# Kernel optimization log

Measured on AMD Instinct MI355X. Metric: run time of the kernel, lower is better.

## Reference

```python
import jax, jax.numpy as jnp
import numpy as np

N, T, D = 32, 64, 16
F = 512  # object_classes == feature dim after object_fc


def _gcn(x, adj, W, b):
    # Kipf GraphConvolution: adj @ (x @ W) + b
    return adj @ (x @ W) + b


def _norm_adj(a):
    d = jnp.sum(a, axis=1) ** -0.5
    return a * d[:, None] * d[None, :]


def _per_graph(x, gc1_W, gc1_b, gc2_W, gc2_b, gc3_W, gc3_b, gc4_W, gc4_b):
    # x: [D, F]
    # graph_generator / adj2: softmax-style similarity adjacency with D^{-1/2} norm
    s = x @ x.T                                   # [D, D]
    a = jnp.exp(s - jnp.max(s, axis=1, keepdims=True))
    adj = _norm_adj(a)
    # branch 1
    x1 = jax.nn.relu(_gcn(x, adj, gc1_W, gc1_b))
    x1 = _gcn(x1, adj, gc2_W, gc2_b)
    # branch 2 (adj_hat2 identical construction from x)
    y2 = jax.nn.relu(_gcn(x, adj, gc3_W, gc3_b))  # [D, 32]
    y22 = y2 @ y2.T
    nrm = jnp.sqrt(jnp.sum(y22 * y22, axis=1, keepdims=True))  # torch.norm(y22, 2, dim=1)
    adj3 = 1.0 + y22 / (nrm @ nrm.T)
    adj_hat3 = _norm_adj(adj3)
    y2 = _gcn(y2, adj_hat3, gc4_W, gc4_b)
    return (x1 + y2) * 0.5


def setup_inputs() -> dict:
    key = jax.random.key(0)
    ks = jax.random.split(key, 12)
    s = 0.02
    return {
        "object_raw": jax.random.normal(ks[0], (N * T * D, F), jnp.float32),
        "action_raw": jax.random.normal(ks[1], (N * T, F), jnp.float32),
        "W_obj": jax.random.normal(ks[2], (F, 512), jnp.float32) * s,
        "b_obj": jnp.zeros((512,), jnp.float32),
        "W_act": jax.random.normal(ks[3], (F, 512), jnp.float32) * s,
        "b_act": jnp.zeros((512,), jnp.float32),
        "gc1_W": jax.random.normal(ks[4], (512, 32), jnp.float32) * s,
        "gc1_b": jnp.zeros((32,), jnp.float32),
        "gc2_W": jax.random.normal(ks[5], (32, 512), jnp.float32) * s,
        "gc2_b": jnp.zeros((512,), jnp.float32),
        "gc3_W": jax.random.normal(ks[6], (512, 32), jnp.float32) * s,
        "gc3_b": jnp.zeros((32,), jnp.float32),
        "gc4_W": jax.random.normal(ks[7], (32, 512), jnp.float32) * s,
        "gc4_b": jnp.zeros((512,), jnp.float32),
        "fc1_W": jax.random.normal(ks[8], (512, 1024), jnp.float32) * s,
        "fc1_b": jnp.zeros((1024,), jnp.float32),
        "clf_W": jax.random.normal(ks[9], (1024, 500), jnp.float32) * s,
        "clf_b": jnp.zeros((500,), jnp.float32),
    }


def reference(object_raw, action_raw, W_obj, b_obj, W_act, b_act,
              gc1_W, gc1_b, gc2_W, gc2_b, gc3_W, gc3_b, gc4_W, gc4_b,
              fc1_W, fc1_b, clf_W, clf_b):
    obj = jax.nn.relu(object_raw @ W_obj + b_obj).reshape(N * T, D, 512)
    act = jax.nn.relu(action_raw @ W_act + b_act)           # [N*T, 512]
    obj = obj.at[:, D // 2].set(act)                         # overwrite middle frame
    graph = jax.vmap(lambda x: _per_graph(x, gc1_W, gc1_b, gc2_W, gc2_b,
                                          gc3_W, gc3_b, gc4_W, gc4_b))(obj)
    g = graph.reshape(N, T, D, 512).mean(axis=2)
    o = obj.reshape(N, T, D, 512).mean(axis=2)
    feat = (o + g) * 0.5                                     # graph_fusion == 'mean'
    c = jax.nn.relu(feat)                                    # dropout = identity (eval)
    c = jax.nn.relu(c @ fc1_W + fc1_b)
    out = (c @ clf_W + clf_b).mean(axis=1)                   # mean over T -> [N, 500]
    return out
```

## Files before the change

kernel.cpp:

```cpp
#include <hip/hip_runtime.h>
#include <hip/hip_bf16.h>

using ushort_t = unsigned short;
using f32x4  = __attribute__((ext_vector_type(4))) float;
using short8 = __attribute__((ext_vector_type(8))) short;

__device__ __forceinline__ float bflo(unsigned p) {
    union { unsigned u; float f; } x; x.u = p << 16; return x.f;
}
__device__ __forceinline__ float bfhi(unsigned p) {
    union { unsigned u; float f; } x; x.u = p & 0xffff0000u; return x.f;
}
__device__ __forceinline__ ushort_t f2bf(float f) {
    __hip_bfloat16 h = __float2bfloat16(f);
    return *(ushort_t*)&h;
}
__device__ __forceinline__ unsigned pk2bf(float lo, float hi) {
    __hip_bfloat162 h = __float22bfloat162_rn({lo, hi});
    return *(unsigned*)&h;
}

typedef __attribute__((address_space(1))) void glb_void;
typedef __attribute__((address_space(3))) void lds_void;
__device__ __forceinline__ void dma16(const void* g, void* l) {
    __builtin_amdgcn_global_load_lds((glb_void*)(unsigned long long)(uintptr_t)g,
                                     (lds_void*)(unsigned)(uintptr_t)l, 16, 0, 0);
}

__device__ __forceinline__ void tr_tile(const float* __restrict__ S, ushort_t* __restrict__ D,
                                        int K, int N, int Npad, int bx, int by,
                                        int tx, int ty, float* tile )
{
    const int k0 = by * 32, n0 = bx * 32;
#pragma unroll
    for (int r = 0; r < 4; r++) {
        const int k = k0 + ty + r * 8, n = n0 + tx;
        tile[(ty + r * 8) * 33 + tx] = (k < K && n < N) ? S[(size_t)k * N + n] : 0.f;
    }
    __syncthreads();
#pragma unroll
    for (int r = 0; r < 4; r++) {
        const int n = n0 + ty + r * 8, k = k0 + tx;
        if (n < Npad && k < K) D[(size_t)n * K + k] = f2bf(tile[tx * 33 + ty + r * 8]);
    }
}

__global__ __launch_bounds__(256)
void prep_weights(const float* __restrict__ Wobj, ushort_t* __restrict__ WobjT,
                  const float* __restrict__ Wact, ushort_t* __restrict__ WactT,
                  const float* __restrict__ fc1W, ushort_t* __restrict__ fc1T,
                  const float* __restrict__ clfW, ushort_t* __restrict__ clfT,
                  const float* __restrict__ gc1W, ushort_t* __restrict__ W1t,
                  const float* __restrict__ gc3W, ushort_t* __restrict__ W3t,
                  const float* __restrict__ gc2W, ushort_t* __restrict__ W2bf,
                  const float* __restrict__ gc4W, ushort_t* __restrict__ W4bf)
{
    __shared__ float tile[32 * 33];
    const int b = blockIdx.x;
    const int t = threadIdx.x;
    const int tx = t & 31, ty = t >> 5;

    if (b < 1568) {
        const float* S; ushort_t* D; int K, N, Npad, nt, l;
        if      (b < 256)  { S = Wobj; D = WobjT; K = 512;  N = 512;  Npad = 512;  nt = 16; l = b; }
        else if (b < 512)  { S = Wact; D = WactT; K = 512;  N = 512;  Npad = 512;  nt = 16; l = b - 256; }
        else if (b < 1024) { S = fc1W; D = fc1T;  K = 512;  N = 1024; Npad = 1024; nt = 32; l = b - 512; }
        else if (b < 1536) { S = clfW; D = clfT;  K = 1024; N = 500;  Npad = 512;  nt = 16; l = b - 1024; }
        else if (b < 1552) { S = gc1W; D = W1t;   K = 512;  N = 32;   Npad = 32;   nt = 1;  l = b - 1536; }
        else               { S = gc3W; D = W3t;   K = 512;  N = 32;   Npad = 32;   nt = 1;  l = b - 1552; }
        tr_tile(S, D, K, N, Npad, l % nt, l / nt, tx, ty, tile);
    } else {
        const float* S = (b < 1576) ? gc2W : gc4W;
        ushort_t* D    = (b < 1576) ? W2bf : W4bf;
        const int i = (b < 1576 ? b - 1568 : b - 1576) * 256 + t;
        const float4 x = ((const float4*)S)[2 * i];
        const float4 y = ((const float4*)S)[2 * i + 1];
        unsigned r[4] = { pk2bf(x.x, x.y), pk2bf(x.z, x.w), pk2bf(y.x, y.y), pk2bf(y.z, y.w) };
        ((uint4*)D)[i] = *(uint4*)r;
    }
}

__device__ __forceinline__ void store_out(ushort_t* C, size_t idx, float v) { C[idx] = f2bf(v); }
__device__ __forceinline__ void store_out(float* C, size_t idx, float v)    { C[idx] = v; }

template<int RELU, typename AT, typename OT>
__device__ __forceinline__ void gemm_core(
    const AT* __restrict__ A, const ushort_t* __restrict__ Bt,
    const float* __restrict__ bias, OT* __restrict__ C,
    int N, int K, int Nb, int row_mul, int row_add, int bm, int bn, int skip8,
    char* AsRaw, ushort_t* Bs)
{
    const int t = threadIdx.x;
    const int lane = t & 63, w = t >> 6;
    const int mb = (w & 1) * 64, nb = (w >> 1) * 64;
    const int fr = lane & 15, fq = lane >> 4;

    f32x4 acc[16];
#pragma unroll
    for (int i = 0; i < 16; i++) acc[i] = (f32x4){0.f, 0.f, 0.f, 0.f};

    const int brow = lane >> 2, bk = lane & 3;
    const int klog = bk ^ ((brow >> 1) & 3);
    const int arow = lane >> 3, ag = lane & 7;

    for (int k0 = 0; k0 < K; k0 += 32) {
        __syncthreads();
        if constexpr (sizeof(AT) == 4) {
#pragma unroll
            for (int i = 0; i < 4; i++) {
                const int grp = w * 4 + i;
                const int row = grp * 8 + arow;
                const int gl = ag ^ (row & 7);
                dma16((const float*)A + (size_t)(bm + row) * K + k0 + gl * 4,
                      AsRaw + grp * 1024);
            }
        } else {
#pragma unroll
            for (int i = 0; i < 2; i++) {
                const int grp = w * 2 + i;
                const int row = grp * 16 + brow;
                dma16((const ushort_t*)A + (size_t)(bm + row) * K + k0 + klog * 8,
                      (ushort_t*)AsRaw + grp * 512);
            }
        }
#pragma unroll
        for (int i = 0; i < 2; i++) {
            const int grp = w * 2 + i;
            const int row = grp * 16 + brow;
            dma16(Bt + (size_t)(bn + row) * K + k0 + klog * 8, Bs + grp * 512);
        }
        __syncthreads();

        short8 af[4], bf[4];
        if constexpr (sizeof(AT) == 4) {
#pragma unroll
            for (int i = 0; i < 4; i++) {
                const int row = mb + i * 16 + fr;
                const float* base = (const float*)AsRaw + row * 32;
                const f32x4 p0 = *(const f32x4*)(base + (((2 * fq)     ^ (fr & 7)) * 4));
                const f32x4 p1 = *(const f32x4*)(base + (((2 * fq + 1) ^ (fr & 7)) * 4));
                unsigned rr[4] = { pk2bf(p0.x, p0.y), pk2bf(p0.z, p0.w),
                                   pk2bf(p1.x, p1.y), pk2bf(p1.z, p1.w) };
                af[i] = *(short8*)rr;
            }
        } else {
#pragma unroll
            for (int i = 0; i < 4; i++) {
                const int row = mb + i * 16 + fr;
                af[i] = *(const short8*)((const ushort_t*)AsRaw + row * 32 + (fq ^ ((fr >> 1) & 3)) * 8);
            }
        }
#pragma unroll
        for (int j = 0; j < 4; j++) {
            const int row = nb + j * 16 + fr;
            bf[j] = *(const short8*)(Bs + row * 32 + (fq ^ ((fr >> 1) & 3)) * 8);
        }
#pragma unroll
        for (int i = 0; i < 4; i++)
#pragma unroll
            for (int j = 0; j < 4; j++)
                acc[i * 4 + j] = __builtin_amdgcn_mfma_f32_16x16x32_bf16(
                    af[i], bf[j], acc[i * 4 + j], 0, 0, 0);
    }

#pragma unroll
    for (int j = 0; j < 4; j++) {
        const int n = bn + nb + j * 16 + fr;
        const float bv = (n < Nb) ? bias[n] : 0.f;
#pragma unroll
        for (int i = 0; i < 4; i++) {
            const f32x4 a = acc[i * 4 + j];
#pragma unroll
            for (int r = 0; r < 4; r++) {
                if (skip8 && (fq * 4 + r) == 8) continue;
                const int m = bm + mb + i * 16 + fq * 4 + r;
                float v = a[r] + bv;
                if (RELU) v = fmaxf(v, 0.f);
                store_out(C, ((size_t)m * row_mul + row_add) * (size_t)N + n, v);
            }
        }
    }
}

__global__ __launch_bounds__(256)
void gemm_objact(const float* __restrict__ Ao, const ushort_t* __restrict__ Bo,
                 const float* __restrict__ bo,
                 const float* __restrict__ Aa, const ushort_t* __restrict__ Ba,
                 const float* __restrict__ ba, ushort_t* __restrict__ C)
{
    __shared__ __align__(16) char     AsRaw[128 * 32 * 4];
    __shared__ __align__(16) ushort_t Bs[128 * 32];
    if (blockIdx.y < 256)
        gemm_core<1, float, ushort_t>(Ao, Bo, bo, C, 512, 512, 512, 1, 0,
                                      blockIdx.y * 128, blockIdx.x * 128, 1, AsRaw, Bs);
    else
        gemm_core<1, float, ushort_t>(Aa, Ba, ba, C, 512, 512, 512, 16, 8,
                                      (blockIdx.y - 256) * 128, blockIdx.x * 128, 0, AsRaw, Bs);
}

template<int RELU, typename AT, typename OT>
__global__ __launch_bounds__(256)
void gemm_dma(const AT* __restrict__ A, const ushort_t* __restrict__ Bt,
              const float* __restrict__ bias, OT* __restrict__ C,
              int N, int K, int Nb, int row_mul, int row_add)
{
    __shared__ __align__(16) char     AsRaw[128 * 32 * sizeof(AT)];
    __shared__ __align__(16) ushort_t Bs[128 * 32];
    gemm_core<RELU, AT, OT>(A, Bt, bias, C, N, K, Nb, row_mul, row_add,
                            blockIdx.y * 128, blockIdx.x * 128, 0, AsRaw, Bs);
}

__global__ __launch_bounds__(64)
void graph_mfma(const ushort_t* __restrict__ obj,
                const ushort_t* __restrict__ W1t, const float* __restrict__ b1,
                const ushort_t* __restrict__ W2b, const float* __restrict__ b2,
                const ushort_t* __restrict__ W3t, const float* __restrict__ b3,
                const ushort_t* __restrict__ W4b, const float* __restrict__ b4,
                ushort_t* __restrict__ cbuf)
{
    __shared__ float ssb[16 * 17];
    __shared__ float adjt[16 * 20];
    __shared__ float t1s[16 * 36];
    __shared__ float t3s[16 * 36];
    __shared__ float x1s[16 * 36];
    __shared__ float y2s[16 * 36];
    __shared__ float y22s[16 * 17];
    __shared__ float a3t[16 * 20];
    __shared__ float dv[16], dv3[16], nrm[16], cA[16], cA3[16];
    __shared__ float zc1[32], zc4[32];

    const int lane = threadIdx.x;
    const int r = lane & 15, fq = lane >> 4;
    const ushort_t* xg = obj + (size_t)blockIdx.x * 8192;

    short8 xf[16];
#pragma unroll
    for (int kk = 0; kk < 16; kk++)
        xf[kk] = *(const short8*)(xg + r * 512 + kk * 32 + fq * 8);

    f32x4 sacc = (f32x4){0.f, 0.f, 0.f, 0.f};
#pragma unroll
    for (int kk = 0; kk < 16; kk++)
        sacc = __builtin_amdgcn_mfma_f32_16x16x32_bf16(xf[kk], xf[kk], sacc, 0, 0, 0);

    f32x4 a10 = (f32x4){0.f,0.f,0.f,0.f}, a11 = a10, a30 = a10, a31 = a10;
#pragma unroll
    for (int kk = 0; kk < 16; kk++) {
        const short8 w10 = *(const short8*)(W1t + (size_t)(r)      * 512 + kk * 32 + fq * 8);
        const short8 w11 = *(const short8*)(W1t + (size_t)(16 + r) * 512 + kk * 32 + fq * 8);
        const short8 w30 = *(const short8*)(W3t + (size_t)(r)      * 512 + kk * 32 + fq * 8);
        const short8 w31 = *(const short8*)(W3t + (size_t)(16 + r) * 512 + kk * 32 + fq * 8);
        a10 = __builtin_amdgcn_mfma_f32_16x16x32_bf16(xf[kk], w10, a10, 0, 0, 0);
        a11 = __builtin_amdgcn_mfma_f32_16x16x32_bf16(xf[kk], w11, a11, 0, 0, 0);
        a30 = __builtin_amdgcn_mfma_f32_16x16x32_bf16(xf[kk], w30, a30, 0, 0, 0);
        a31 = __builtin_amdgcn_mfma_f32_16x16x32_bf16(xf[kk], w31, a31, 0, 0, 0);
    }

#pragma unroll
    for (int i = 0; i < 4; i++) {
        const int m = fq * 4 + i;
        ssb[m * 17 + r] = sacc[i];
        t1s[m * 36 + r]      = a10[i];
        t1s[m * 36 + 16 + r] = a11[i];
        t3s[m * 36 + r]      = a30[i];
        t3s[m * 36 + 16 + r] = a31[i];
    }
    __syncthreads();

    if (lane < 16) {
        float m = ssb[lane * 17];
#pragma unroll
        for (int j = 1; j < 16; j++) m = fmaxf(m, ssb[lane * 17 + j]);
        float s = 0.f;
#pragma unroll
        for (int j = 0; j < 16; j++) {
            const float e = expf(ssb[lane * 17 + j] - m);
            ssb[lane * 17 + j] = e; s += e;
        }
        dv[lane] = rsqrtf(s);
    }
    __syncthreads();

    {
        const float di = dv[r];
#pragma unroll
        for (int p = 0; p < 4; p++) {
            const int j = fq * 4 + p;
            adjt[j * 20 + r] = ssb[r * 17 + j] * di * dv[j];
        }
    }
    __syncthreads();

    if (lane < 16) {
        float s = 0.f;
#pragma unroll
        for (int i = 0; i < 16; i++) s += adjt[lane * 20 + i];
        cA[lane] = s;
    }

    {
        const int c = lane & 31, hi = lane >> 5;
        const float bb1 = b1[c], bb3 = b3[c];
        float ax[8], ay[8];
#pragma unroll
        for (int i = 0; i < 8; i++) { ax[i] = bb1; ay[i] = bb3; }
#pragma unroll
        for (int j = 0; j < 16; j++) {
            const float t1v = t1s[j * 36 + c], t3v = t3s[j * 36 + c];
            const float4 p = *(const float4*)&adjt[j * 20 + hi * 8];
            const float4 q = *(const float4*)&adjt[j * 20 + hi * 8 + 4];
            ax[0] = fmaf(p.x, t1v, ax[0]); ax[1] = fmaf(p.y, t1v, ax[1]);
            ax[2] = fmaf(p.z, t1v, ax[2]); ax[3] = fmaf(p.w, t1v, ax[3]);
            ax[4] = fmaf(q.x, t1v, ax[4]); ax[5] = fmaf(q.y, t1v, ax[5]);
            ax[6] = fmaf(q.z, t1v, ax[6]); ax[7] = fmaf(q.w, t1v, ax[7]);
            ay[0] = fmaf(p.x, t3v, ay[0]); ay[1] = fmaf(p.y, t3v, ay[1]);
            ay[2] = fmaf(p.z, t3v, ay[2]); ay[3] = fmaf(p.w, t3v, ay[3]);
            ay[4] = fmaf(q.x, t3v, ay[4]); ay[5] = fmaf(q.y, t3v, ay[5]);
            ay[6] = fmaf(q.z, t3v, ay[6]); ay[7] = fmaf(q.w, t3v, ay[7]);
        }
#pragma unroll
        for (int i = 0; i < 8; i++) {
            x1s[(hi * 8 + i) * 36 + c] = fmaxf(ax[i], 0.f);
            y2s[(hi * 8 + i) * 36 + c] = fmaxf(ay[i], 0.f);
        }
    }
    __syncthreads();

    {
        const int i2 = lane >> 2, j0 = (lane & 3) * 4;
        float a4[4] = {0.f, 0.f, 0.f, 0.f};
#pragma unroll
        for (int k4 = 0; k4 < 8; k4++) {
            const float4 yi = *(const float4*)&y2s[i2 * 36 + k4 * 4];
#pragma unroll
            for (int p = 0; p < 4; p++) {
                const float4 yj = *(const float4*)&y2s[(j0 + p) * 36 + k4 * 4];
                a4[p] = fmaf(yi.x, yj.x, a4[p]); a4[p] = fmaf(yi.y, yj.y, a4[p]);
                a4[p] = fmaf(yi.z, yj.z, a4[p]); a4[p] = fmaf(yi.w, yj.w, a4[p]);
            }
        }
#pragma unroll
        for (int p = 0; p < 4; p++) y22s[i2 * 17 + j0 + p] = a4[p];
    }
    __syncthreads();

    if (lane < 16) {
        float sq = 0.f;
#pragma unroll
        for (int j = 0; j < 16; j++) { const float v = y22s[lane * 17 + j]; sq = fmaf(v, v, sq); }
        nrm[lane] = sqrtf(sq);
    }
    __syncthreads();

    {
        const float ni = nrm[r];
#pragma unroll
        for (int p = 0; p < 4; p++) {
            const int j = fq * 4 + p;
            a3t[j * 20 + r] = 1.0f + y22s[r * 17 + j] / (ni * nrm[j]);
        }
    }
    __syncthreads();

    if (lane < 16) {
        float s = 0.f;
#pragma unroll
        for (int j = 0; j < 16; j++) s += a3t[j * 20 + lane];
        dv3[lane] = rsqrtf(s);
    }
    __syncthreads();

    if (lane < 16) {
        float s = 0.f;
#pragma unroll
        for (int i = 0; i < 16; i++) s = fmaf(a3t[lane * 20 + i], dv3[i], s);
        cA3[lane] = s * dv3[lane];
    }
    __syncthreads();

    if (lane < 32) {
        float s1 = 0.f, s4 = 0.f;
#pragma unroll
        for (int j = 0; j < 16; j++) {
            s1 = fmaf(cA[j],  x1s[j * 36 + lane], s1);
            s4 = fmaf(cA3[j], y2s[j * 36 + lane], s4);
        }
        zc1[lane] = s1; zc4[lane] = s4;
    }
    __syncthreads();

    {
        float om[8] = {0,0,0,0,0,0,0,0};
#pragma unroll
        for (int m = 0; m < 16; m++) {
            const uint4 q = *(const uint4*)(xg + m * 512 + lane * 8);
            om[0] += bflo(q.x); om[1] += bfhi(q.x);
            om[2] += bflo(q.y); om[3] += bfhi(q.y);
            om[4] += bflo(q.z); om[5] += bfhi(q.z);
            om[6] += bflo(q.w); om[7] += bfhi(q.w);
        }
        float gm[8] = {0,0,0,0,0,0,0,0};
        for (int k = 0; k < 32; k++) {
            const float z1 = zc1[k], z4 = zc4[k];
            const uint4 w2 = *(const uint4*)(W2b + (size_t)k * 512 + lane * 8);
            const uint4 w4 = *(const uint4*)(W4b + (size_t)k * 512 + lane * 8);
            gm[0] = fmaf(z1, bflo(w2.x), gm[0]); gm[0] = fmaf(z4, bflo(w4.x), gm[0]);
            gm[1] = fmaf(z1, bfhi(w2.x), gm[1]); gm[1] = fmaf(z4, bfhi(w4.x), gm[1]);
            gm[2] = fmaf(z1, bflo(w2.y), gm[2]); gm[2] = fmaf(z4, bflo(w4.y), gm[2]);
            gm[3] = fmaf(z1, bfhi(w2.y), gm[3]); gm[3] = fmaf(z4, bfhi(w4.y), gm[3]);
            gm[4] = fmaf(z1, bflo(w2.z), gm[4]); gm[4] = fmaf(z4, bflo(w4.z), gm[4]);
            gm[5] = fmaf(z1, bfhi(w2.z), gm[5]); gm[5] = fmaf(z4, bfhi(w4.z), gm[5]);
            gm[6] = fmaf(z1, bflo(w2.w), gm[6]); gm[6] = fmaf(z4, bflo(w4.w), gm[6]);
            gm[7] = fmaf(z1, bfhi(w2.w), gm[7]); gm[7] = fmaf(z4, bfhi(w4.w), gm[7]);
        }
        const float4 b2a = *(const float4*)&b2[lane * 8];
        const float4 b2b = *(const float4*)&b2[lane * 8 + 4];
        const float4 b4a = *(const float4*)&b4[lane * 8];
        const float4 b4b = *(const float4*)&b4[lane * 8 + 4];
        const float bs[8] = { b2a.x + b4a.x, b2a.y + b4a.y, b2a.z + b4a.z, b2a.w + b4a.w,
                              b2b.x + b4b.x, b2b.y + b4b.y, b2b.z + b4b.z, b2b.w + b4b.w };
        ushort_t pk[8];
#pragma unroll
        for (int c = 0; c < 8; c++) {
            const float gmean = 0.5f * bs[c] + gm[c] * (1.0f / 32.0f);
            const float feat  = 0.5f * (om[c] * 0.0625f + gmean);
            pk[c] = f2bf(fmaxf(feat, 0.f));
        }
        *(uint4*)(cbuf + (size_t)blockIdx.x * 512 + lane * 8) = *(uint4*)pk;
    }
}

__global__ __launch_bounds__(256)
void mean_c2(const ushort_t* __restrict__ c2, float* __restrict__ cmean)
{
    const int idx = blockIdx.x * 256 + threadIdx.x;
    const int n = idx >> 10, k = idx & 1023;
    const ushort_t* p = c2 + (size_t)n * 64 * 1024 + k;
    float s = 0.f;
#pragma unroll 8
    for (int tt = 0; tt < 64; tt++) {
        union { unsigned u; float f; } x; x.u = ((unsigned)p[tt * 1024]) << 16;
        s += x.f;
    }
    cmean[idx] = s * (1.0f / 64.0f);
}

__global__ __launch_bounds__(256)
void clf_small(const float* __restrict__ cmean, const ushort_t* __restrict__ clfT,
               const float* __restrict__ clf_b, float* __restrict__ out)
{
    const int t = threadIdx.x;
    const int n = t & 31, jo = t >> 5;
    const int j = blockIdx.x * 8 + jo;
    const float4* cm = (const float4*)(cmean + (size_t)n * 1024);
    const uint2*  wr = (const uint2*)(clfT + (size_t)(j < 500 ? j : 499) * 1024);
    float acc = 0.f;
#pragma unroll 4
    for (int k4 = 0; k4 < 256; k4++) {
        const float4 c = cm[k4];
        const uint2  w = wr[k4];
        acc = fmaf(c.x, bflo(w.x), acc);
        acc = fmaf(c.y, bfhi(w.x), acc);
        acc = fmaf(c.z, bflo(w.y), acc);
        acc = fmaf(c.w, bfhi(w.y), acc);
    }
    if (j < 500) out[(size_t)n * 500 + j] = acc + clf_b[j];
}

extern "C" void kernel_launch(void* const* d_in, const int* in_sizes, int n_in,
                              void* d_out, int out_size, void* d_ws, size_t ws_size,
                              hipStream_t stream)
{
    const float* object_raw = (const float*)d_in[0];
    const float* action_raw = (const float*)d_in[1];
    const float* W_obj = (const float*)d_in[2];
    const float* b_obj = (const float*)d_in[3];
    const float* W_act = (const float*)d_in[4];
    const float* b_act = (const float*)d_in[5];
    const float* gc1_W = (const float*)d_in[6];
    const float* gc1_b = (const float*)d_in[7];
    const float* gc2_W = (const float*)d_in[8];
    const float* gc2_b = (const float*)d_in[9];
    const float* gc3_W = (const float*)d_in[10];
    const float* gc3_b = (const float*)d_in[11];
    const float* gc4_W = (const float*)d_in[12];
    const float* gc4_b = (const float*)d_in[13];
    const float* fc1_W = (const float*)d_in[14];
    const float* fc1_b = (const float*)d_in[15];
    const float* clf_W = (const float*)d_in[16];
    const float* clf_b = (const float*)d_in[17];

    char* ws = (char*)d_ws;
    const size_t MB = 1024 * 1024;
    ushort_t* obj_bf = (ushort_t*)(ws);
    ushort_t* cbuf   = (ushort_t*)(ws + 32 * MB);
    ushort_t* c2     = (ushort_t*)(ws + 34 * MB);
    float*    cmean  = (float*)   (ws + 38 * MB);
    ushort_t* WobjT  = (ushort_t*)(ws + 39 * MB);
    ushort_t* WactT  = (ushort_t*)(ws + 39 * MB + 512 * 1024);
    ushort_t* fc1T   = (ushort_t*)(ws + 40 * MB);
    ushort_t* clfT   = (ushort_t*)(ws + 41 * MB);
    ushort_t* W1t    = (ushort_t*)(ws + 42 * MB);
    ushort_t* W3t    = (ushort_t*)(ws + 42 * MB + 32 * 1024);
    ushort_t* W2bf   = (ushort_t*)(ws + 42 * MB + 64 * 1024);
    ushort_t* W4bf   = (ushort_t*)(ws + 42 * MB + 96 * 1024);

    prep_weights<<<dim3(1584), 256, 0, stream>>>(
        W_obj, WobjT, W_act, WactT, fc1_W, fc1T, clf_W, clfT,
        gc1_W, W1t, gc3_W, W3t, gc2_W, W2bf, gc4_W, W4bf);

    gemm_objact<<<dim3(4, 272), 256, 0, stream>>>(
        object_raw, WobjT, b_obj, action_raw, WactT, b_act, obj_bf);

    graph_mfma<<<dim3(2048), 64, 0, stream>>>(
        obj_bf, W1t, gc1_b, W2bf, gc2_b, W3t, gc3_b, W4bf, gc4_b, cbuf);

    gemm_dma<1, ushort_t, ushort_t><<<dim3(8, 16), 256, 0, stream>>>(
        cbuf, fc1T, fc1_b, c2, 1024, 512, 1024, 1, 0);

    mean_c2<<<dim3(128), 256, 0, stream>>>(c2, cmean);

    clf_small<<<dim3(63), 256, 0, stream>>>(cmean, clfT, clf_b, (float*)d_out);
}
```

Before: 267.5 us.

## Stream full-K object rows into LDS and compute all 512 columns per block

Replaces the fused object/action GEMM with a dedicated object GEMM. Each block converts a 64x512 fp32 A tile to bf16 once into swizzled LDS, then computes all 512 output columns, streaming B from global memory into registers with double buffering. This removes the fourfold re-read of the large fp32 object matrix across column tiles and the per-k-step LDS synchronisation. The action GEMM moves to a separate launch, which adds a small kernel and uses a large LDS footprint (64 KB per block).

```diff
diff --git a/kernel.cpp b/kernel.cpp
--- a/kernel.cpp
+++ b/kernel.cpp
@@ -18,13 +18,6 @@
 __device__ __forceinline__ unsigned pk2bf(float lo, float hi) {
     __hip_bfloat162 h = __float22bfloat162_rn({lo, hi});
     return *(unsigned*)&h;
-}
-
-typedef __attribute__((address_space(1))) void glb_void;
-typedef __attribute__((address_space(3))) void lds_void;
-__device__ __forceinline__ void dma16(const void* g, void* l) {
-    __builtin_amdgcn_global_load_lds((glb_void*)(unsigned long long)(uintptr_t)g,
-                                     (lds_void*)(unsigned)(uintptr_t)l, 16, 0, 0);
 }
 
 __device__ __forceinline__ void tr_tile(const float* __restrict__ S, ushort_t* __restrict__ D,
@@ -80,18 +73,106 @@
     }
 }
 
+__global__ __launch_bounds__(256, 2)
+void gemm_obj_stream(const float* __restrict__ A, const ushort_t* __restrict__ Bt,
+                     const float* __restrict__ bias, ushort_t* __restrict__ C)
+{
+    __shared__ __align__(16) ushort_t As[64 * 512];
+    const int t = threadIdx.x;
+    const int lane = t & 63, w = t >> 6;
+    const int bm = blockIdx.x * 64;
+    const int fr = lane & 15, fq = lane >> 4;
+
+#pragma unroll
+    for (int i = 0; i < 16; i++) {
+        const int flat = i * 256 + t;
+        const int row = flat >> 6, c = flat & 63;
+        const float* gp = A + (size_t)(bm + row) * 512 + c * 8;
+        const float4 p0 = *(const float4*)gp;
+        const float4 p1 = *(const float4*)(gp + 4);
+        unsigned rr[4] = { pk2bf(p0.x, p0.y), pk2bf(p0.z, p0.w),
+                           pk2bf(p1.x, p1.y), pk2bf(p1.z, p1.w) };
+        *(uint4*)&As[row * 512 + ((c ^ (row & 7)) * 8)] = *(uint4*)rr;
+    }
+    __syncthreads();
+
+    const int nw = w * 128;
+    const ushort_t* Bbase = Bt + (size_t)(nw + fr) * 512 + fq * 8;
+
+    f32x4 acc[8][4];
+#pragma unroll
+    for (int j = 0; j < 8; j++)
+#pragma unroll
+        for (int i = 0; i < 4; i++) acc[j][i] = (f32x4){0.f, 0.f, 0.f, 0.f};
+
+    uint4 bA[8], bB[8];
+#pragma unroll
+    for (int j = 0; j < 8; j++) bA[j] = *(const uint4*)(Bbase + (size_t)j * 16 * 512);
+
+    for (int kk = 0; kk < 16; kk += 2) {
+        short8 af[4];
+#pragma unroll
+        for (int i = 0; i < 4; i++)
+            af[i] = *(const short8*)&As[(i * 16 + fr) * 512 + (((kk * 4 + fq) ^ (fr & 7)) * 8)];
+#pragma unroll
+        for (int j = 0; j < 8; j++) {
+            bB[j] = *(const uint4*)(Bbase + (size_t)j * 16 * 512 + (kk + 1) * 32);
+            const short8 bf = *(const short8*)&bA[j];
+#pragma unroll
+            for (int i = 0; i < 4; i++)
+                acc[j][i] = __builtin_amdgcn_mfma_f32_16x16x32_bf16(af[i], bf, acc[j][i], 0, 0, 0);
+        }
+#pragma unroll
+        for (int i = 0; i < 4; i++)
+            af[i] = *(const short8*)&As[(i * 16 + fr) * 512 + ((((kk + 1) * 4 + fq) ^ (fr & 7)) * 8)];
+#pragma unroll
+        for (int j = 0; j < 8; j++) {
+            if (kk + 2 < 16)
+                bA[j] = *(const uint4*)(Bbase + (size_t)j * 16 * 512 + (kk + 2) * 32);
+            const short8 bf = *(const short8*)&bB[j];
+#pragma unroll
+            for (int i = 0; i < 4; i++)
+                acc[j][i] = __builtin_amdgcn_mfma_f32_16x16x32_bf16(af[i], bf, acc[j][i], 0, 0, 0);
+        }
+    }
+
+#pragma unroll
+    for (int j = 0; j < 8; j++) {
+        const int n = nw + j * 16 + fr;
+        const float bv = bias[n];
+#pragma unroll
+        for (int i = 0; i < 4; i++) {
+#pragma unroll
+            for (int rr = 0; rr < 4; rr++) {
+                const int ml = fq * 4 + rr;
+                if (ml == 8) continue;
+                const int m = bm + i * 16 + ml;
+                C[(size_t)m * 512 + n] = f2bf(fmaxf(acc[j][i][rr] + bv, 0.f));
+            }
+        }
+    }
+}
+
+typedef __attribute__((address_space(1))) void glb_void;
+typedef __attribute__((address_space(3))) void lds_void;
+__device__ __forceinline__ void dma16(const void* g, void* l) {
+    __builtin_amdgcn_global_load_lds((glb_void*)(unsigned long long)(uintptr_t)g,
+                                     (lds_void*)(unsigned)(uintptr_t)l, 16, 0, 0);
+}
 __device__ __forceinline__ void store_out(ushort_t* C, size_t idx, float v) { C[idx] = f2bf(v); }
 __device__ __forceinline__ void store_out(float* C, size_t idx, float v)    { C[idx] = v; }
 
 template<int RELU, typename AT, typename OT>
-__device__ __forceinline__ void gemm_core(
-    const AT* __restrict__ A, const ushort_t* __restrict__ Bt,
-    const float* __restrict__ bias, OT* __restrict__ C,
-    int N, int K, int Nb, int row_mul, int row_add, int bm, int bn, int skip8,
-    char* AsRaw, ushort_t* Bs)
-{
+__global__ __launch_bounds__(256)
+void gemm_dma(const AT* __restrict__ A, const ushort_t* __restrict__ Bt,
+              const float* __restrict__ bias, OT* __restrict__ C,
+              int N, int K, int Nb, int row_mul, int row_add)
+{
+    __shared__ __align__(16) char     AsRaw[128 * 32 * sizeof(AT)];
+    __shared__ __align__(16) ushort_t Bs[128 * 32];
     const int t = threadIdx.x;
     const int lane = t & 63, w = t >> 6;
+    const int bm = blockIdx.y * 128, bn = blockIdx.x * 128;
     const int mb = (w & 1) * 64, nb = (w >> 1) * 64;
     const int fr = lane & 15, fq = lane >> 4;
 
@@ -172,7 +253,6 @@
             const f32x4 a = acc[i * 4 + j];
 #pragma unroll
             for (int r = 0; r < 4; r++) {
-                if (skip8 && (fq * 4 + r) == 8) continue;
                 const int m = bm + mb + i * 16 + fq * 4 + r;
                 float v = a[r] + bv;
                 if (RELU) v = fmaxf(v, 0.f);
@@ -180,34 +260,6 @@
             }
         }
     }
-}
-
-__global__ __launch_bounds__(256)
-void gemm_objact(const float* __restrict__ Ao, const ushort_t* __restrict__ Bo,
-                 const float* __restrict__ bo,
-                 const float* __restrict__ Aa, const ushort_t* __restrict__ Ba,
-                 const float* __restrict__ ba, ushort_t* __restrict__ C)
-{
-    __shared__ __align__(16) char     AsRaw[128 * 32 * 4];
-    __shared__ __align__(16) ushort_t Bs[128 * 32];
-    if (blockIdx.y < 256)
-        gemm_core<1, float, ushort_t>(Ao, Bo, bo, C, 512, 512, 512, 1, 0,
-                                      blockIdx.y * 128, blockIdx.x * 128, 1, AsRaw, Bs);
-    else
-        gemm_core<1, float, ushort_t>(Aa, Ba, ba, C, 512, 512, 512, 16, 8,
-                                      (blockIdx.y - 256) * 128, blockIdx.x * 128, 0, AsRaw, Bs);
-}
-
-template<int RELU, typename AT, typename OT>
-__global__ __launch_bounds__(256)
-void gemm_dma(const AT* __restrict__ A, const ushort_t* __restrict__ Bt,
-              const float* __restrict__ bias, OT* __restrict__ C,
-              int N, int K, int Nb, int row_mul, int row_add)
-{
-    __shared__ __align__(16) char     AsRaw[128 * 32 * sizeof(AT)];
-    __shared__ __align__(16) ushort_t Bs[128 * 32];
-    gemm_core<RELU, AT, OT>(A, Bt, bias, C, N, K, Nb, row_mul, row_add,
-                            blockIdx.y * 128, blockIdx.x * 128, 0, AsRaw, Bs);
 }
 
 __global__ __launch_bounds__(64)
@@ -509,8 +561,10 @@
         W_obj, WobjT, W_act, WactT, fc1_W, fc1T, clf_W, clfT,
         gc1_W, W1t, gc3_W, W3t, gc2_W, W2bf, gc4_W, W4bf);
 
-    gemm_objact<<<dim3(4, 272), 256, 0, stream>>>(
-        object_raw, WobjT, b_obj, action_raw, WactT, b_act, obj_bf);
+    gemm_obj_stream<<<dim3(512), 256, 0, stream>>>(object_raw, WobjT, b_obj, obj_bf);
+
+    gemm_dma<1, float, ushort_t><<<dim3(4, 16), 256, 0, stream>>>(
+        action_raw, WactT, b_act, obj_bf, 512, 512, 512, 16, 8);
 
     graph_mfma<<<dim3(2048), 64, 0, stream>>>(
         obj_bf, W1t, gc1_b, W2bf, gc2_b, W3t, gc3_b, W4bf, gc4_b, cbuf);
```

New measurement: 268.9 us. Within noise of the previous version (+0.5%).
